# Performance work log

Hardware: AMD Instinct MI355X
Metric: run time of the kernel (lower is better)

## Reference

```python
import jax, jax.numpy as jnp
import numpy as np
from jax import lax

B, C, H, W = 32, 512, 56, 56
CO = 512
EPS = 1e-5

def binarize(x):
    # sign binarization with hardtanh straight-through estimator (BNN 1w1a)
    xc = jnp.clip(x, -1.0, 1.0)
    return xc + lax.stop_gradient(jnp.sign(x) - xc)

def batchnorm(y, g, b, m, v):
    # inference-mode BN with running stats, per-channel over NCHW
    inv = g * lax.rsqrt(v + EPS)
    return y * inv[None, :, None, None] + (b - m * inv)[None, :, None, None]

def setup_inputs() -> dict:
    key = jax.random.key(0)
    ks = jax.random.split(key, 11)
    return {
        "x": jax.random.normal(ks[0], (B, C, H, W), dtype=jnp.float32),
        "w_dw": jax.random.normal(ks[1], (C, 1, 3, 3), dtype=jnp.float32),
        "w_pw": jax.random.normal(ks[2], (CO, C, 1, 1), dtype=jnp.float32),
        "g1": jax.random.uniform(ks[3], (C,), dtype=jnp.float32),
        "b1": jax.random.normal(ks[4], (C,), dtype=jnp.float32),
        "m1": jax.random.normal(ks[5], (C,), dtype=jnp.float32),
        "v1": jax.random.uniform(ks[6], (C,), dtype=jnp.float32),
        "g2": jax.random.uniform(ks[7], (CO,), dtype=jnp.float32),
        "b2": jax.random.normal(ks[8], (CO,), dtype=jnp.float32),
        "m2": jax.random.normal(ks[9], (CO,), dtype=jnp.float32),
        "v2": jax.random.uniform(ks[10], (CO,), dtype=jnp.float32),
    }

def reference(x, w_dw, w_pw, g1, b1, m1, v1, g2, b2, m2, v2):
    dn = ('NCHW', 'OIHW', 'NCHW')
    # binary depthwise 3x3, stride 1, pad 1, groups=C
    out = lax.conv_general_dilated(
        binarize(x), binarize(w_dw), window_strides=(1, 1),
        padding=((1, 1), (1, 1)), feature_group_count=C,
        dimension_numbers=dn)
    out = batchnorm(out, g1, b1, m1, v1)
    # binary pointwise 1x1
    out = lax.conv_general_dilated(
        binarize(out), binarize(w_pw), window_strides=(1, 1),
        padding=((0, 0), (0, 0)), dimension_numbers=dn)
    out = batchnorm(out, g2, b2, m2, v2)
    return out
```

## Files before the change

kernel.cpp:

```cpp
#include <hip/hip_runtime.h>

#define BB 32
#define CC 512
#define COO 512
#define HH 56
#define WW 56
#define HW 3136
#define NPOS 100352
#define EPSF 1e-5f

typedef unsigned long long u64;
typedef unsigned int u32;
typedef unsigned short u16;

#define OFF_S1      0
#define OFF_WBITS   6422528
#define OFF_WN      6455296
#define OFF_NT      6455872
#define OFF_BN2INV  6456832
#define OFF_BN2BETA 6458880

__global__ __launch_bounds__(256) void setup_kernel(
    const float* __restrict__ w_dw, const float* __restrict__ w_pw,
    const float* __restrict__ g1, const float* __restrict__ b1,
    const float* __restrict__ m1, const float* __restrict__ v1,
    const float* __restrict__ g2, const float* __restrict__ b2,
    const float* __restrict__ m2, const float* __restrict__ v2,
    u64* __restrict__ wbits, u64* __restrict__ wn, u64* __restrict__ NT,
    float* __restrict__ bn2inv, float* __restrict__ bn2beta) {
    const int t = blockIdx.x * 256 + threadIdx.x;

    {
        int o = t >> 3, wi = t & 7;
        const float* wp = w_pw + (size_t)o * CC + wi * 64;
        u64 wrd = 0;
        #pragma unroll 8
        for (int k = 0; k < 64; ++k)
            wrd |= (u64)(wp[k] >= 0.f) << k;
        wbits[t] = wrd;
    }

    if (t < CC) {
        float i2 = g2[t] / sqrtf(v2[t] + EPSF);
        bn2inv[t]  = i2;
        bn2beta[t] = b2[t] - m2[t] * i2;
    } else if (t >= 512 && t < 584) {
        int q = t - 512, cw = q & 7, tap = q >> 3;
        u64 wv = 0;
        for (int cl = 0; cl < 64; ++cl)
            wv |= (u64)(w_dw[(size_t)(cw * 64 + cl) * 9 + tap] < 0.f) << cl;
        wn[tap * 8 + cw] = wv;
    } else if (t >= 1024 && t < 1048) {
        int q = t - 1024, cat = q / 8, cw = q % 8;
        const int Nv = (cat == 0) ? 9 : ((cat == 1) ? 6 : 4);
        u64 p0 = 0, p1 = 0, p2 = 0, p3 = 0, F = 0;
        for (int cl = 0; cl < 64; ++cl) {
            int c = cw * 64 + cl;
            float i1 = g1[c] / sqrtf(v1[c] + EPSF);
            float be = b1[c] - m1[c] * i1;
            int T, f;
            if (i1 > 0.f) {
                double h = ((double)Nv - (double)be / (double)i1) * 0.5;
                f = 0;
                if (!(h > 0.0)) T = 0;
                else if (h > 15.0) T = 15;
                else T = (int)ceil(h);
            } else if (i1 < 0.f) {
                double h = ((double)Nv - (double)be / (double)i1) * 0.5;
                f = 1;
                if (h < 0.0) T = 0;
                else if (h >= 15.0) T = 15;
                else { T = (int)floor(h) + 1; if (T > 15) T = 15; }
            } else {
                f = 0;
                T = (be >= 0.f) ? 0 : 15;
            }
            unsigned nt = (~(unsigned)T) & 0xFu;
            p0 |= (u64)(nt & 1) << cl;
            p1 |= (u64)((nt >> 1) & 1) << cl;
            p2 |= (u64)((nt >> 2) & 1) << cl;
            p3 |= (u64)((nt >> 3) & 1) << cl;
            F  |= (u64)f << cl;
        }
        u64* d = NT + (size_t)(cat * 8 + cw) * 5;
        d[0] = p0; d[1] = p1; d[2] = p2; d[3] = p3; d[4] = F;
    }
}

__device__ __forceinline__ void fa(u64 a, u64 b, u64 c, u64& s, u64& cy) {
    u64 ab = a ^ b;
    s  = ab ^ c;
    cy = (ab & c) | (a & b);
}

__global__ __launch_bounds__(256) void dwfused_kernel(
    const float* __restrict__ x, const u64* __restrict__ wn,
    const u64* __restrict__ NT, u64* __restrict__ s1) {
    __shared__ u64 xb[16 * 56];
    const int strip = blockIdx.x;
    const int cw    = blockIdx.y;
    const int b     = blockIdx.z;
    const int tid   = threadIdx.x;
    const int r0    = strip * 14;

    const float* xc = x + ((size_t)b * CC + cw * 64) * HW;
    u16* xb16 = (u16*)xb;

    for (int tau = tid; tau < 896; tau += 256) {
        const int lrow   = tau / 56;
        const int rest   = tau - lrow * 56;
        const int colgrp = rest >> 2, cg = rest & 3;
        const int h      = r0 - 1 + lrow;
        const int col0   = colgrp * 4;
        u16 o0 = 0, o1 = 0, o2 = 0, o3 = 0;
        if (h >= 0 && h < HH) {
            const float* bp = xc + (size_t)(cg * 16) * HW + h * WW + col0;
            u32 a0 = 0, a1 = 0, a2 = 0, a3 = 0;
            #pragma unroll
            for (int cl = 0; cl < 16; ++cl) {
                float4 v = *(const float4*)(bp + (size_t)cl * HW);
                a0 |= (__float_as_uint(v.x) >> 31) << cl;
                a1 |= (__float_as_uint(v.y) >> 31) << cl;
                a2 |= (__float_as_uint(v.z) >> 31) << cl;
                a3 |= (__float_as_uint(v.w) >> 31) << cl;
            }
            o0 = (u16)(~a0); o1 = (u16)(~a1); o2 = (u16)(~a2); o3 = (u16)(~a3);
        }
        const int wbase = lrow * 56 + col0;
        xb16[(wbase + 0) * 4 + cg] = o0;
        xb16[(wbase + 1) * 4 + cg] = o1;
        xb16[(wbase + 2) * 4 + cg] = o2;
        xb16[(wbase + 3) * 4 + cg] = o3;
    }
    __syncthreads();

    if (tid >= 196) return;
    const int q      = tid / 14;
    const int colgrp = tid - q * 14;
    const int col0   = colgrp * 4;
    const int r      = r0 + q;
    const int lrow   = q + 1;

    const int c_m1 = (col0 == 0)  ? 0  : col0 - 1;
    const int c_p4 = (col0 == 52) ? 55 : col0 + 4;

    const u64* rowT = xb + (lrow - 1) * 56;
    const u64* rowM = xb + lrow * 56;
    const u64* rowB = xb + (lrow + 1) * 56;

    u64 rT[6], rM[6], rB[6];
    rT[0] = rowT[c_m1]; rT[1] = rowT[col0];   rT[2] = rowT[col0+1];
    rT[3] = rowT[col0+2]; rT[4] = rowT[col0+3]; rT[5] = rowT[c_p4];
    rM[0] = rowM[c_m1]; rM[1] = rowM[col0];   rM[2] = rowM[col0+1];
    rM[3] = rowM[col0+2]; rM[4] = rowM[col0+3]; rM[5] = rowM[c_p4];
    rB[0] = rowB[c_m1]; rB[1] = rowB[col0];   rB[2] = rowB[col0+1];
    rB[3] = rowB[col0+2]; rB[4] = rowB[col0+3]; rB[5] = rowB[c_p4];

    const u64 w00 = wn[0*8+cw], w01 = wn[1*8+cw], w02 = wn[2*8+cw];
    const u64 w10 = wn[3*8+cw], w11 = wn[4*8+cw], w12 = wn[5*8+cw];
    const u64 w20 = wn[6*8+cw], w21 = wn[7*8+cw], w22 = wn[8*8+cw];

    const u64 mt = (r > 0)    ? ~0ull : 0ull;
    const u64 mb = (r < 55)   ? ~0ull : 0ull;
    const u64 mL = (col0 > 0) ? ~0ull : 0ull;
    const u64 mR = (col0 < 52)? ~0ull : 0ull;

    const bool rowe = (r == 0) || (r == 55);
    const u64* NTc = NT + (size_t)cw * 5;
    u64 A0 = rowe ? NTc[40+0] : NTc[0];
    u64 A1 = rowe ? NTc[40+1] : NTc[1];
    u64 A2 = rowe ? NTc[40+2] : NTc[2];
    u64 A3 = rowe ? NTc[40+3] : NTc[3];
    u64 A4 = rowe ? NTc[40+4] : NTc[4];
    u64 B0 = rowe ? NTc[80+0] : NTc[40+0];
    u64 B1 = rowe ? NTc[80+1] : NTc[40+1];
    u64 B2 = rowe ? NTc[80+2] : NTc[40+2];
    u64 B3 = rowe ? NTc[80+3] : NTc[40+3];
    u64 B4 = rowe ? NTc[80+4] : NTc[40+4];

    u64 out[4];
    #pragma unroll
    for (int j = 0; j < 4; ++j) {
        u64 e0 = (rT[j]   ^ w00) & mt;
        u64 e1 = (rT[j+1] ^ w01) & mt;
        u64 e2 = (rT[j+2] ^ w02) & mt;
        u64 e3 = (rM[j]   ^ w10);
        u64 e4 = (rM[j+1] ^ w11);
        u64 e5 = (rM[j+2] ^ w12);
        u64 e6 = (rB[j]   ^ w20) & mb;
        u64 e7 = (rB[j+1] ^ w21) & mb;
        u64 e8 = (rB[j+2] ^ w22) & mb;
        if (j == 0) { e0 &= mL; e3 &= mL; e6 &= mL; }
        if (j == 3) { e2 &= mR; e5 &= mR; e8 &= mR; }

        u64 sa, ca, sb, cb, sc, cc, E0, cd, se, ce;
        fa(e0, e1, e2, sa, ca);
        fa(e3, e4, e5, sb, cb);
        fa(e6, e7, e8, sc, cc);
        fa(sa, sb, sc, E0, cd);
        fa(ca, cb, cc, se, ce);
        u64 E1 = se ^ cd, cf = se & cd;
        u64 E2 = ce ^ cf, E3 = ce & cf;

        u64 n0, n1, n2, n3, Fv;
        if (j == 0) {
            u64 m = (col0 == 0) ? ~0ull : 0ull;
            n0 = (B0 & m) | (A0 & ~m); n1 = (B1 & m) | (A1 & ~m);
            n2 = (B2 & m) | (A2 & ~m); n3 = (B3 & m) | (A3 & ~m);
            Fv = (B4 & m) | (A4 & ~m);
        } else if (j == 3) {
            u64 m = (col0 == 52) ? ~0ull : 0ull;
            n0 = (B0 & m) | (A0 & ~m); n1 = (B1 & m) | (A1 & ~m);
            n2 = (B2 & m) | (A2 & ~m); n3 = (B3 & m) | (A3 & ~m);
            Fv = (B4 & m) | (A4 & ~m);
        } else {
            n0 = A0; n1 = A1; n2 = A2; n3 = A3; Fv = A4;
        }

        u64 c = E0 | n0;
        c = (E1 & n1) | (c & (E1 | n1));
        c = (E2 & n2) | (c & (E2 | n2));
        c = (E3 & n3) | (c & (E3 | n3));
        out[j] = c ^ Fv;
    }

    u64* sp = s1 + (size_t)cw * NPOS + (size_t)b * HW + r * WW + col0;
    *(ulonglong2*)(sp)     = make_ulonglong2(out[0], out[1]);
    *(ulonglong2*)(sp + 2) = make_ulonglong2(out[2], out[3]);
}

__global__ __launch_bounds__(256) void pw_kernel(
    const u64* __restrict__ s1, const u64* __restrict__ wbits,
    const float* __restrict__ bn2inv, const float* __restrict__ bn2beta,
    float* __restrict__ out) {
    __shared__ u64  wb[128 * 8];
    __shared__ float inv_s[128], beta_s[128];
    const int tid = threadIdx.x;
    const int o0  = blockIdx.y * 128;

    for (int i = tid; i < 1024; i += 256) wb[i] = wbits[(size_t)o0 * 8 + i];
    if (tid < 128) { inv_s[tid] = bn2inv[o0 + tid]; beta_s[tid] = bn2beta[o0 + tid]; }
    __syncthreads();

    const size_t p   = (size_t)blockIdx.x * 256 + tid;
    const int    b   = (int)(p / HW);
    const int    idx = (int)(p - (size_t)b * HW);

    u64 r0 = s1[0u * NPOS + p], r1 = s1[1u * NPOS + p];
    u64 r2 = s1[2u * NPOS + p], r3 = s1[3u * NPOS + p];
    u64 r4 = s1[4u * NPOS + p], r5 = s1[5u * NPOS + p];
    u64 r6 = s1[6u * NPOS + p], r7 = s1[7u * NPOS + p];

    float* outp = out + ((size_t)b * COO) * HW + idx;

    for (int ol = 0; ol < 128; ++ol) {
        const u64* w8 = wb + ol * 8;
        int d = __popcll(r0 ^ w8[0]) + __popcll(r1 ^ w8[1])
              + __popcll(r2 ^ w8[2]) + __popcll(r3 ^ w8[3])
              + __popcll(r4 ^ w8[4]) + __popcll(r5 ^ w8[5])
              + __popcll(r6 ^ w8[6]) + __popcll(r7 ^ w8[7]);
        float res = (float)(CC - 2 * d);
        outp[(size_t)(o0 + ol) * HW] = fmaf(res, inv_s[ol], beta_s[ol]);
    }
}

extern "C" void kernel_launch(void* const* d_in, const int* in_sizes, int n_in,
                              void* d_out, int out_size, void* d_ws, size_t ws_size,
                              hipStream_t stream) {
    const float* x    = (const float*)d_in[0];
    const float* w_dw = (const float*)d_in[1];
    const float* w_pw = (const float*)d_in[2];
    const float* g1   = (const float*)d_in[3];
    const float* b1   = (const float*)d_in[4];
    const float* m1   = (const float*)d_in[5];
    const float* v1   = (const float*)d_in[6];
    const float* g2   = (const float*)d_in[7];
    const float* b2   = (const float*)d_in[8];
    const float* m2   = (const float*)d_in[9];
    const float* v2   = (const float*)d_in[10];

    char* ws = (char*)d_ws;
    u64*   s1      = (u64*)(ws + OFF_S1);
    u64*   wbits   = (u64*)(ws + OFF_WBITS);
    u64*   wn      = (u64*)(ws + OFF_WN);
    u64*   NTarr   = (u64*)(ws + OFF_NT);
    float* bn2inv  = (float*)(ws + OFF_BN2INV);
    float* bn2beta = (float*)(ws + OFF_BN2BETA);

    setup_kernel<<<16, 256, 0, stream>>>(w_dw, w_pw, g1, b1, m1, v1, g2, b2, m2, v2,
                                         wbits, wn, NTarr, bn2inv, bn2beta);

    dim3 gf(4, 8, BB);
    dwfused_kernel<<<gf, 256, 0, stream>>>(x, wn, NTarr, s1);

    dim3 g2d(392, 4);
    pw_kernel<<<g2d, 256, 0, stream>>>(s1, wbits, bn2inv, bn2beta, (float*)d_out);
}
```

Before: 154.2 us.

## Use one thread per pixel in depthwise kernel and read pointwise weights from global

The depthwise kernel now launches 512 threads per block. Each thread computes one output pixel instead of four, so far more threads are busy after the shared-memory staging. The edge-case correction table is now indexed by a combined row/column edge count. The pointwise kernel drops its shared-memory staging of weights and BN parameters and reads them straight from global memory as uniform scalar loads, with a 4-way unroll. The trade-off is more redundant neighbour loads from shared memory and scattered 8-byte stores in the depthwise kernel, and the pointwise loop now depends on cache hits for its weight loads.

New measurement: 154.4 us. No clear change (+0.1%).

```diff
diff --git a/kernel.cpp b/kernel.cpp
--- a/kernel.cpp
+++ b/kernel.cpp
@@ -93,7 +93,7 @@
     cy = (ab & c) | (a & b);
 }
 
-__global__ __launch_bounds__(256) void dwfused_kernel(
+__global__ __launch_bounds__(512) void dwfused_kernel(
     const float* __restrict__ x, const u64* __restrict__ wn,
     const u64* __restrict__ NT, u64* __restrict__ s1) {
     __shared__ u64 xb[16 * 56];
@@ -106,7 +106,7 @@
     const float* xc = x + ((size_t)b * CC + cw * 64) * HW;
     u16* xb16 = (u16*)xb;
 
-    for (int tau = tid; tau < 896; tau += 256) {
+    for (int tau = tid; tau < 896; tau += 512) {
         const int lrow   = tau / 56;
         const int rest   = tau - lrow * 56;
         const int colgrp = rest >> 2, cg = rest & 3;
@@ -134,64 +134,39 @@
     }
     __syncthreads();
 
-    if (tid >= 196) return;
-    const int q      = tid / 14;
-    const int colgrp = tid - q * 14;
-    const int col0   = colgrp * 4;
-    const int r      = r0 + q;
-    const int lrow   = q + 1;
-
-    const int c_m1 = (col0 == 0)  ? 0  : col0 - 1;
-    const int c_p4 = (col0 == 52) ? 55 : col0 + 4;
-
-    const u64* rowT = xb + (lrow - 1) * 56;
-    const u64* rowM = xb + lrow * 56;
-    const u64* rowB = xb + (lrow + 1) * 56;
-
-    u64 rT[6], rM[6], rB[6];
-    rT[0] = rowT[c_m1]; rT[1] = rowT[col0];   rT[2] = rowT[col0+1];
-    rT[3] = rowT[col0+2]; rT[4] = rowT[col0+3]; rT[5] = rowT[c_p4];
-    rM[0] = rowM[c_m1]; rM[1] = rowM[col0];   rM[2] = rowM[col0+1];
-    rM[3] = rowM[col0+2]; rM[4] = rowM[col0+3]; rM[5] = rowM[c_p4];
-    rB[0] = rowB[c_m1]; rB[1] = rowB[col0];   rB[2] = rowB[col0+1];
-    rB[3] = rowB[col0+2]; rB[4] = rowB[col0+3]; rB[5] = rowB[c_p4];
-
     const u64 w00 = wn[0*8+cw], w01 = wn[1*8+cw], w02 = wn[2*8+cw];
     const u64 w10 = wn[3*8+cw], w11 = wn[4*8+cw], w12 = wn[5*8+cw];
     const u64 w20 = wn[6*8+cw], w21 = wn[7*8+cw], w22 = wn[8*8+cw];
 
-    const u64 mt = (r > 0)    ? ~0ull : 0ull;
-    const u64 mb = (r < 55)   ? ~0ull : 0ull;
-    const u64 mL = (col0 > 0) ? ~0ull : 0ull;
-    const u64 mR = (col0 < 52)? ~0ull : 0ull;
-
-    const bool rowe = (r == 0) || (r == 55);
-    const u64* NTc = NT + (size_t)cw * 5;
-    u64 A0 = rowe ? NTc[40+0] : NTc[0];
-    u64 A1 = rowe ? NTc[40+1] : NTc[1];
-    u64 A2 = rowe ? NTc[40+2] : NTc[2];
-    u64 A3 = rowe ? NTc[40+3] : NTc[3];
-    u64 A4 = rowe ? NTc[40+4] : NTc[4];
-    u64 B0 = rowe ? NTc[80+0] : NTc[40+0];
-    u64 B1 = rowe ? NTc[80+1] : NTc[40+1];
-    u64 B2 = rowe ? NTc[80+2] : NTc[40+2];
-    u64 B3 = rowe ? NTc[80+3] : NTc[40+3];
-    u64 B4 = rowe ? NTc[80+4] : NTc[40+4];
-
-    u64 out[4];
-    #pragma unroll
-    for (int j = 0; j < 4; ++j) {
-        u64 e0 = (rT[j]   ^ w00) & mt;
-        u64 e1 = (rT[j+1] ^ w01) & mt;
-        u64 e2 = (rT[j+2] ^ w02) & mt;
-        u64 e3 = (rM[j]   ^ w10);
-        u64 e4 = (rM[j+1] ^ w11);
-        u64 e5 = (rM[j+2] ^ w12);
-        u64 e6 = (rB[j]   ^ w20) & mb;
-        u64 e7 = (rB[j+1] ^ w21) & mb;
-        u64 e8 = (rB[j+2] ^ w22) & mb;
-        if (j == 0) { e0 &= mL; e3 &= mL; e6 &= mL; }
-        if (j == 3) { e2 &= mR; e5 &= mR; e8 &= mR; }
+    for (int task = tid; task < 784; task += 512) {
+        const int q = task / 56;
+        const int c = task - q * 56;
+        const int r = r0 + q;
+        const int lrow = q + 1;
+        const int cm = (c == 0)  ? 0  : c - 1;
+        const int cp = (c == 55) ? 55 : c + 1;
+
+        const u64* rT = xb + (lrow - 1) * 56;
+        const u64* rM = xb + lrow * 56;
+        const u64* rB = xb + (lrow + 1) * 56;
+        u64 t0 = rT[cm], t1 = rT[c], t2 = rT[cp];
+        u64 m0 = rM[cm], m1 = rM[c], m2 = rM[cp];
+        u64 b0 = rB[cm], b1 = rB[c], b2 = rB[cp];
+
+        const u64 mt = (r > 0)  ? ~0ull : 0ull;
+        const u64 mb = (r < 55) ? ~0ull : 0ull;
+        const u64 ml = (c > 0)  ? ~0ull : 0ull;
+        const u64 mr = (c < 55) ? ~0ull : 0ull;
+
+        u64 e0 = (t0 ^ w00) & mt & ml;
+        u64 e1 = (t1 ^ w01) & mt;
+        u64 e2 = (t2 ^ w02) & mt & mr;
+        u64 e3 = (m0 ^ w10) & ml;
+        u64 e4 = (m1 ^ w11);
+        u64 e5 = (m2 ^ w12) & mr;
+        u64 e6 = (b0 ^ w20) & mb & ml;
+        u64 e7 = (b1 ^ w21) & mb;
+        u64 e8 = (b2 ^ w22) & mb & mr;
 
         u64 sa, ca, sb, cb, sc, cc, E0, cd, se, ce;
         fa(e0, e1, e2, sa, ca);
@@ -202,45 +177,26 @@
         u64 E1 = se ^ cd, cf = se & cd;
         u64 E2 = ce ^ cf, E3 = ce & cf;
 
-        u64 n0, n1, n2, n3, Fv;
-        if (j == 0) {
-            u64 m = (col0 == 0) ? ~0ull : 0ull;
-            n0 = (B0 & m) | (A0 & ~m); n1 = (B1 & m) | (A1 & ~m);
-            n2 = (B2 & m) | (A2 & ~m); n3 = (B3 & m) | (A3 & ~m);
-            Fv = (B4 & m) | (A4 & ~m);
-        } else if (j == 3) {
-            u64 m = (col0 == 52) ? ~0ull : 0ull;
-            n0 = (B0 & m) | (A0 & ~m); n1 = (B1 & m) | (A1 & ~m);
-            n2 = (B2 & m) | (A2 & ~m); n3 = (B3 & m) | (A3 & ~m);
-            Fv = (B4 & m) | (A4 & ~m);
-        } else {
-            n0 = A0; n1 = A1; n2 = A2; n3 = A3; Fv = A4;
-        }
-
-        u64 c = E0 | n0;
-        c = (E1 & n1) | (c & (E1 | n1));
-        c = (E2 & n2) | (c & (E2 | n2));
-        c = (E3 & n3) | (c & (E3 | n3));
-        out[j] = c ^ Fv;
-    }
-
-    u64* sp = s1 + (size_t)cw * NPOS + (size_t)b * HW + r * WW + col0;
-    *(ulonglong2*)(sp)     = make_ulonglong2(out[0], out[1]);
-    *(ulonglong2*)(sp + 2) = make_ulonglong2(out[2], out[3]);
+        const int rowe = (r == 0) | (r == 55);
+        const int cole = (c == 0) | (c == 55);
+        const u64* NTp = NT + (size_t)(rowe + cole) * 40 + (size_t)cw * 5;
+        u64 n0 = NTp[0], n1 = NTp[1], n2 = NTp[2], n3 = NTp[3], Fv = NTp[4];
+
+        u64 cr = E0 | n0;
+        cr = (E1 & n1) | (cr & (E1 | n1));
+        cr = (E2 & n2) | (cr & (E2 | n2));
+        cr = (E3 & n3) | (cr & (E3 | n3));
+
+        s1[(size_t)cw * NPOS + (size_t)b * HW + r * WW + c] = cr ^ Fv;
+    }
 }
 
 __global__ __launch_bounds__(256) void pw_kernel(
     const u64* __restrict__ s1, const u64* __restrict__ wbits,
     const float* __restrict__ bn2inv, const float* __restrict__ bn2beta,
     float* __restrict__ out) {
-    __shared__ u64  wb[128 * 8];
-    __shared__ float inv_s[128], beta_s[128];
     const int tid = threadIdx.x;
     const int o0  = blockIdx.y * 128;
-
-    for (int i = tid; i < 1024; i += 256) wb[i] = wbits[(size_t)o0 * 8 + i];
-    if (tid < 128) { inv_s[tid] = bn2inv[o0 + tid]; beta_s[tid] = bn2beta[o0 + tid]; }
-    __syncthreads();
 
     const size_t p   = (size_t)blockIdx.x * 256 + tid;
     const int    b   = (int)(p / HW);
@@ -251,16 +207,20 @@
     u64 r4 = s1[4u * NPOS + p], r5 = s1[5u * NPOS + p];
     u64 r6 = s1[6u * NPOS + p], r7 = s1[7u * NPOS + p];
 
-    float* outp = out + ((size_t)b * COO) * HW + idx;
-
+    const u64*   wp  = wbits + (size_t)o0 * 8;
+    const float* ivp = bn2inv + o0;
+    const float* btp = bn2beta + o0;
+    float* outp = out + ((size_t)b * COO + o0) * HW + idx;
+
+    #pragma unroll 4
     for (int ol = 0; ol < 128; ++ol) {
-        const u64* w8 = wb + ol * 8;
+        const u64* w8 = wp + ol * 8;
         int d = __popcll(r0 ^ w8[0]) + __popcll(r1 ^ w8[1])
               + __popcll(r2 ^ w8[2]) + __popcll(r3 ^ w8[3])
               + __popcll(r4 ^ w8[4]) + __popcll(r5 ^ w8[5])
               + __popcll(r6 ^ w8[6]) + __popcll(r7 ^ w8[7]);
         float res = (float)(CC - 2 * d);
-        outp[(size_t)(o0 + ol) * HW] = fmaf(res, inv_s[ol], beta_s[ol]);
+        outp[(size_t)ol * HW] = fmaf(res, ivp[ol], btp[ol]);
     }
 }
 
@@ -291,7 +251,7 @@
                                          wbits, wn, NTarr, bn2inv, bn2beta);
 
     dim3 gf(4, 8, BB);
-    dwfused_kernel<<<gf, 256, 0, stream>>>(x, wn, NTarr, s1);
+    dwfused_kernel<<<gf, 512, 0, stream>>>(x, wn, NTarr, s1);
 
     dim3 g2d(392, 4);
     pw_kernel<<<g2d, 256, 0, stream>>>(s1, wbits, bn2inv, bn2beta, (float*)d_out);
```
